# Optimization experiments

Hardware: AMD Instinct MI355X
Metric: run time of the kernel (lower is better)

The kernel has to match this reference:

```python
import jax, jax.numpy as jnp
import numpy as np

N_NODES = 20000  # number of batch nodes (static for segment ops)

def setup_inputs() -> dict:
    key = jax.random.key(0)
    N, E, V, D = N_NODES, 640000, 100000, 64
    ks = jax.random.split(key, 8)
    nodes = jax.random.randint(ks[0], (N,), 0, V)
    neigh_idx = jax.random.randint(ks[1], (E,), 0, V)
    seg_ids = jnp.sort(jax.random.randint(ks[2], (E,), 0, N))  # ragged degrees, sorted by node
    u2e = jax.random.normal(ks[3], (V, D), jnp.float32) * 0.02
    s1 = 1.0 / np.sqrt(2 * D)
    s2 = 1.0 / np.sqrt(D)
    att1_w = jax.random.uniform(ks[4], (2 * D, D), jnp.float32, -s1, s1)
    att1_b = jnp.zeros((D,), jnp.float32)
    att2_w = jax.random.uniform(ks[5], (D, D), jnp.float32, -s2, s2)
    att2_b = jnp.zeros((D,), jnp.float32)
    att3_w = jax.random.uniform(ks[6], (D, 1), jnp.float32, -s2, s2)
    att3_b = jnp.zeros((1,), jnp.float32)
    return dict(nodes=nodes, neigh_idx=neigh_idx, seg_ids=seg_ids, u2e=u2e,
                att1_w=att1_w, att1_b=att1_b, att2_w=att2_w, att2_b=att2_b,
                att3_w=att3_w, att3_b=att3_b)


def reference(nodes, neigh_idx, seg_ids, u2e, att1_w, att1_b, att2_w, att2_b, att3_w, att3_b):
    # Ragged per-node neighbor attention, flattened over all edges.
    e_u = u2e[neigh_idx]              # [E, D] neighbor embeddings
    u_rep = u2e[nodes][seg_ids]       # [E, D] center-node embedding broadcast per edge
    x = jnp.concatenate([e_u, u_rep], axis=1)            # [E, 2D]
    x = jax.nn.relu(x @ att1_w + att1_b)                  # [E, D]
    x = jax.nn.relu(x @ att2_w + att2_b)                  # [E, D]
    logits = (x @ att3_w + att3_b)[:, 0]                  # [E]
    # segment softmax over each node's neighbor set
    m = jax.ops.segment_max(logits, seg_ids, num_segments=N_NODES)
    m = jnp.where(jnp.isfinite(m), m, 0.0)                # guard empty segments
    ex = jnp.exp(logits - m[seg_ids])
    denom = jax.ops.segment_sum(ex, seg_ids, num_segments=N_NODES)
    att = ex / jnp.maximum(denom[seg_ids], 1e-9)          # [E]
    # attention-weighted sum of neighbor embeddings per node (e_u^T @ att_w per node)
    out = jax.ops.segment_sum(att[:, None] * e_u, seg_ids, num_segments=N_NODES)  # [N, D]
    return out
```

## Files before the change

### kernel.cpp

```cpp
#include <hip/hip_runtime.h>
#include <hip/hip_bf16.h>

typedef __attribute__((ext_vector_type(8))) short bf16x8;
typedef __attribute__((ext_vector_type(4))) float f32x4;

__device__ __forceinline__ unsigned short f2bf(float f) {
    unsigned x = __float_as_uint(f);
    unsigned r = (x + 0x7FFF + ((x >> 16) & 1)) >> 16;
    return (unsigned short)r;
}
__device__ __forceinline__ bf16x8 cvt8(const float* __restrict__ p) {
    bf16x8 r;
#pragma unroll
    for (int j = 0; j < 8; ++j) r[j] = (short)f2bf(p[j]);
    return r;
}
__device__ __forceinline__ unsigned pack_relu_bf16(unsigned yv, unsigned zv) {
    float lo = fmaxf(__uint_as_float(yv << 16) + __uint_as_float(zv << 16), 0.0f);
    float hi = fmaxf(__uint_as_float(yv & 0xFFFF0000u) + __uint_as_float(zv & 0xFFFF0000u), 0.0f);
    __hip_bfloat162 p = __float22bfloat162_rn(float2{lo, hi});
    return *(unsigned*)&p;
}

template <bool T1>
__launch_bounds__(256)
__global__ void conv_all_k(const float* __restrict__ u2e,
                           const int* __restrict__ nodes,
                           const int* __restrict__ segs,
                           const float* __restrict__ w1,
                           const float* __restrict__ w2,
                           const float* __restrict__ b1f,
                           unsigned short* __restrict__ yu,
                           unsigned short* __restrict__ z,
                           unsigned short* __restrict__ w2t,
                           int* __restrict__ seg_off,
                           float* __restrict__ zout,
                           float* __restrict__ den,
                           int V, int N, int E, int yblk, int zblk,
                           int ytiles, int ztiles) {
    __shared__ __align__(16) unsigned short w1l[64 * 72];
    const int bid = blockIdx.x;
    const int t = threadIdx.x;
    const int wid = t >> 6;
    const int lane = t & 63;
    const int q = lane >> 4;
    const int m15 = lane & 15;

    if (bid < yblk + zblk) {
        const bool isY = bid < yblk;
        const int kbase = isY ? 0 : 64;
        for (int u = t; u < 64 * 16; u += 256) {
            int k = u >> 4;
            int n4 = (u & 15) * 4;
            float4 v = *(const float4*)(w1 + (long)(kbase + k) * 64 + n4);
            w1l[(n4 + 0) * 72 + k] = f2bf(v.x);
            w1l[(n4 + 1) * 72 + k] = f2bf(v.y);
            w1l[(n4 + 2) * 72 + k] = f2bf(v.z);
            w1l[(n4 + 3) * 72 + k] = f2bf(v.w);
        }
        __syncthreads();

        bf16x8 wb0[4], wb1[4];
#pragma unroll
        for (int b = 0; b < 4; ++b) {
            const unsigned short* wr = w1l + (b * 16 + m15) * 72;
            wb0[b] = *(const bf16x8*)(wr + q * 8);
            wb1[b] = *(const bf16x8*)(wr + 32 + q * 8);
        }

        if (isY) {
            const int ystride = T1 ? 128 : 64;
            for (int tile = bid; tile < ytiles; tile += yblk) {
                const int wbase = tile * 64 + wid * 16;
                if (wbase >= V) continue;
                int row = min(wbase + m15, V - 1);
                const float* p = u2e + (long)row * 64;
                bf16x8 a0 = cvt8(p + q * 8);
                bf16x8 a1 = cvt8(p + 32 + q * 8);
                if (T1 && wbase + m15 < V) {
                    *(bf16x8*)(yu + (long)row * 128 + 64 + q * 8) = a0;
                    *(bf16x8*)(yu + (long)row * 128 + 96 + q * 8) = a1;
                }
                f32x4 acc[4];
#pragma unroll
                for (int b = 0; b < 4; ++b) {
                    acc[b] = (f32x4){0.f, 0.f, 0.f, 0.f};
                    acc[b] = __builtin_amdgcn_mfma_f32_16x16x32_bf16(a0, wb0[b], acc[b], 0, 0, 0);
                    acc[b] = __builtin_amdgcn_mfma_f32_16x16x32_bf16(a1, wb1[b], acc[b], 0, 0, 0);
                }
#pragma unroll
                for (int b = 0; b < 4; ++b)
#pragma unroll
                    for (int r = 0; r < 4; ++r) {
                        int rr = wbase + q * 4 + r;
                        if (rr < V) yu[(long)rr * ystride + b * 16 + m15] = f2bf(acc[b][r]);
                    }
            }
        } else {
            float b1v[4];
#pragma unroll
            for (int b = 0; b < 4; ++b) b1v[b] = b1f[b * 16 + m15];
            for (int tile = bid - yblk; tile < ztiles; tile += zblk) {
                const int wbase = tile * 64 + wid * 16;
                if (wbase >= N) continue;
                int nd = nodes[min(wbase + m15, N - 1)];
                const float* p = u2e + (long)nd * 64;
                bf16x8 a0 = cvt8(p + q * 8);
                bf16x8 a1 = cvt8(p + 32 + q * 8);
                f32x4 acc[4];
#pragma unroll
                for (int b = 0; b < 4; ++b) {
                    acc[b] = (f32x4){b1v[b], b1v[b], b1v[b], b1v[b]};
                    acc[b] = __builtin_amdgcn_mfma_f32_16x16x32_bf16(a0, wb0[b], acc[b], 0, 0, 0);
                    acc[b] = __builtin_amdgcn_mfma_f32_16x16x32_bf16(a1, wb1[b], acc[b], 0, 0, 0);
                }
#pragma unroll
                for (int b = 0; b < 4; ++b)
#pragma unroll
                    for (int r = 0; r < 4; ++r) {
                        int rr = wbase + q * 4 + r;
                        if (rr < N) z[(long)rr * 64 + b * 16 + m15] = f2bf(acc[b][r]);
                    }
            }
        }
    } else if (bid == yblk + zblk) {
        for (int i = t; i < 64 * 64; i += 256) {
            int k = i >> 6, n = i & 63;
            w2t[n * 64 + k] = f2bf(w2[i]);
        }
    } else {
        if (T1) {
            long zt = (long)(bid - yblk - zblk - 1) * 256 + t;
            long nth = (long)(gridDim.x - yblk - zblk - 1) * 256;
            f32x4 zz = (f32x4){0.f, 0.f, 0.f, 0.f};
            for (long i = zt; i < (long)N * 16; i += nth) ((f32x4*)zout)[i] = zz;
            for (long i = zt; i < (long)((N + 3) / 4); i += nth) ((f32x4*)den)[i] = zz;
        } else {
            int idx = (bid - yblk - zblk - 1) * 256 + t;
            if (idx > N) return;
            int l = 0, r = E;
            while (l < r) { int mid = (l + r) >> 1; if (segs[mid] < idx) l = mid + 1; else r = mid; }
            seg_off[idx] = l;
        }
    }
}

__launch_bounds__(256)
__global__ void fused_ea_k(const int* __restrict__ neigh,
                           const int* __restrict__ segs,
                           const unsigned short* __restrict__ yu,
                           const unsigned short* __restrict__ z,
                           const unsigned short* __restrict__ w2t,
                           const float* __restrict__ b2f,
                           const float* __restrict__ w3f,
                           const float* __restrict__ b3f,
                           float* __restrict__ outp,
                           float* __restrict__ den, int E) {
    const int wid = threadIdx.x >> 6;
    const int lane = threadIdx.x & 63;
    const int q = lane >> 4;
    const int m15 = lane & 15;
    const long base = ((long)blockIdx.x * 4 + wid) * 32;
    if (base >= E) return;

    int vi[2], sg[2];
    bool val[2];
#pragma unroll
    for (int g = 0; g < 2; ++g) {
        long e = base + g * 16 + m15;
        val[g] = e < E;
        int ec = (int)(val[g] ? e : (long)E - 1);
        vi[g] = neigh[ec];
        sg[g] = segs[ec];
    }
    bf16x8 y0[2], y1[2], u0[2], u1[2], zz0[2], zz1[2];
#pragma unroll
    for (int g = 0; g < 2; ++g) {
        const unsigned short* r = yu + (long)vi[g] * 128;
        y0[g] = *(const bf16x8*)(r + q * 8);
        y1[g] = *(const bf16x8*)(r + 32 + q * 8);
        u0[g] = *(const bf16x8*)(r + 64 + q * 16);
        u1[g] = *(const bf16x8*)(r + 64 + q * 16 + 8);
        const unsigned short* zr = z + (long)sg[g] * 64;
        zz0[g] = *(const bf16x8*)(zr + q * 8);
        zz1[g] = *(const bf16x8*)(zr + 32 + q * 8);
    }

    float b2v[4], w3v[4];
#pragma unroll
    for (int b = 0; b < 4; ++b) {
        b2v[b] = b2f[b * 16 + m15];
        w3v[b] = w3f[b * 16 + m15];
    }
    const float b3v = b3f[0];

    f32x4 acc[2][4];
#pragma unroll
    for (int g = 0; g < 2; ++g) {
        bf16x8 h0, h1;
#pragma unroll
        for (int j = 0; j < 4; ++j) {
            ((unsigned*)&h0)[j] = pack_relu_bf16(((unsigned*)&y0[g])[j], ((unsigned*)&zz0[g])[j]);
            ((unsigned*)&h1)[j] = pack_relu_bf16(((unsigned*)&y1[g])[j], ((unsigned*)&zz1[g])[j]);
        }
#pragma unroll
        for (int b = 0; b < 4; ++b) {
            acc[g][b] = (f32x4){b2v[b], b2v[b], b2v[b], b2v[b]};
            const bf16x8* wrow = (const bf16x8*)(w2t + (b * 16 + m15) * 64);
            acc[g][b] = __builtin_amdgcn_mfma_f32_16x16x32_bf16(h0, wrow[0 + q], acc[g][b], 0, 0, 0);
            acc[g][b] = __builtin_amdgcn_mfma_f32_16x16x32_bf16(h1, wrow[4 + q], acc[g][b], 0, 0, 0);
        }
    }

#pragma unroll
    for (int g = 0; g < 2; ++g) {
        float ev[4];
#pragma unroll
        for (int r = 0; r < 4; ++r) {
            float v = 0.0f;
#pragma unroll
            for (int b = 0; b < 4; ++b) v += fmaxf(acc[g][b][r], 0.0f) * w3v[b];
            v += __shfl_xor(v, 1);
            v += __shfl_xor(v, 2);
            v += __shfl_xor(v, 4);
            v += __shfl_xor(v, 8);
            ev[r] = __expf(v + b3v);
        }
        int rsel = m15 & 3;
        float exval = rsel == 0 ? ev[0] : (rsel == 1 ? ev[1] : (rsel == 2 ? ev[2] : ev[3]));
        float exm = __shfl(exval, ((m15 >> 2) << 4) | (m15 & 3));
        if (!val[g]) exm = 0.0f;

        float uc[16];
        const unsigned* du0 = (const unsigned*)&u0[g];
        const unsigned* du1 = (const unsigned*)&u1[g];
#pragma unroll
        for (int tt = 0; tt < 4; ++tt) {
            uc[2 * tt]         = __uint_as_float(du0[tt] << 16);
            uc[2 * tt + 1]     = __uint_as_float(du0[tt] & 0xFFFF0000u);
            uc[8 + 2 * tt]     = __uint_as_float(du1[tt] << 16);
            uc[8 + 2 * tt + 1] = __uint_as_float(du1[tt] & 0xFFFF0000u);
        }

        const int ndlo = __shfl(sg[g], 0);
        const int ndhi = __shfl(sg[g], 15);
        for (int nd = ndlo; nd <= ndhi; ++nd) {
            float sel = (sg[g] == nd) ? exm : 0.0f;
            float cs[16];
#pragma unroll
            for (int c = 0; c < 16; ++c) cs[c] = sel * uc[c];
            float c8[8];
            {
                const bool b = m15 & 1;
#pragma unroll
                for (int i = 0; i < 8; ++i) {
                    float keep = b ? cs[2 * i + 1] : cs[2 * i];
                    float send = b ? cs[2 * i] : cs[2 * i + 1];
                    c8[i] = keep + __shfl_xor(send, 1);
                }
            }
            float c4[4];
            {
                const bool b = m15 & 2;
#pragma unroll
                for (int i = 0; i < 4; ++i) {
                    float keep = b ? c8[2 * i + 1] : c8[2 * i];
                    float send = b ? c8[2 * i] : c8[2 * i + 1];
                    c4[i] = keep + __shfl_xor(send, 2);
                }
            }
            float c2[2];
            {
                const bool b = m15 & 4;
#pragma unroll
                for (int i = 0; i < 2; ++i) {
                    float keep = b ? c4[2 * i + 1] : c4[2 * i];
                    float send = b ? c4[2 * i] : c4[2 * i + 1];
                    c2[i] = keep + __shfl_xor(send, 4);
                }
            }
            float tot;
            {
                const bool b = m15 & 8;
                float keep = b ? c2[1] : c2[0];
                float send = b ? c2[0] : c2[1];
                tot = keep + __shfl_xor(send, 8);
            }
            atomicAdd(outp + (long)nd * 64 + lane, tot);
            float ds = sel;
            ds += __shfl_xor(ds, 1);
            ds += __shfl_xor(ds, 2);
            ds += __shfl_xor(ds, 4);
            ds += __shfl_xor(ds, 8);
            if (lane == 0) atomicAdd(den + nd, ds);
        }
    }
}

__launch_bounds__(256)
__global__ void div_k(float* __restrict__ out, const float* __restrict__ den, int N) {
    int i = blockIdx.x * 256 + threadIdx.x;
    if (i >= N * 16) return;
    float inv = 1.0f / fmaxf(den[i >> 4], 1e-9f);
    f32x4* p = (f32x4*)out + i;
    f32x4 v = *p;
    v[0] *= inv; v[1] *= inv; v[2] *= inv; v[3] *= inv;
    *p = v;
}

__launch_bounds__(256)
__global__ void logits2_k(const int* __restrict__ neigh,
                          const int* __restrict__ segs,
                          const unsigned short* __restrict__ Y,
                          const unsigned short* __restrict__ z,
                          const unsigned short* __restrict__ w2t,
                          const float* __restrict__ b2f,
                          const float* __restrict__ w3f, const float* __restrict__ b3f,
                          float* __restrict__ ex, int E) {
    const int wid = threadIdx.x >> 6;
    const int lane = threadIdx.x & 63;
    const int q = lane >> 4;
    const int m15 = lane & 15;
    const long base = ((long)blockIdx.x * 4 + wid) * 32;
    if (base >= E) return;

    int vi[2], sg[2];
#pragma unroll
    for (int g = 0; g < 2; ++g) {
        long e = base + g * 16 + m15;
        int ec = (int)(e < E ? e : (long)E - 1);
        vi[g] = neigh[ec];
        sg[g] = segs[ec];
    }
    bf16x8 y0[2], y1[2], zz0[2], zz1[2];
#pragma unroll
    for (int g = 0; g < 2; ++g) {
        const unsigned short* yr = Y + (long)vi[g] * 64;
        y0[g] = *(const bf16x8*)(yr + q * 8);
        y1[g] = *(const bf16x8*)(yr + 32 + q * 8);
        const unsigned short* zr = z + (long)sg[g] * 64;
        zz0[g] = *(const bf16x8*)(zr + q * 8);
        zz1[g] = *(const bf16x8*)(zr + 32 + q * 8);
    }

    float b2v[4], w3v[4];
#pragma unroll
    for (int b = 0; b < 4; ++b) {
        b2v[b] = b2f[b * 16 + m15];
        w3v[b] = w3f[b * 16 + m15];
    }

    f32x4 acc[2][4];
#pragma unroll
    for (int g = 0; g < 2; ++g) {
        bf16x8 h0, h1;
#pragma unroll
        for (int j = 0; j < 4; ++j) {
            ((unsigned*)&h0)[j] = pack_relu_bf16(((unsigned*)&y0[g])[j], ((unsigned*)&zz0[g])[j]);
            ((unsigned*)&h1)[j] = pack_relu_bf16(((unsigned*)&y1[g])[j], ((unsigned*)&zz1[g])[j]);
        }
#pragma unroll
        for (int b = 0; b < 4; ++b) {
            acc[g][b] = (f32x4){b2v[b], b2v[b], b2v[b], b2v[b]};
            const bf16x8* wrow = (const bf16x8*)(w2t + (b * 16 + m15) * 64);
            acc[g][b] = __builtin_amdgcn_mfma_f32_16x16x32_bf16(h0, wrow[0 + q], acc[g][b], 0, 0, 0);
            acc[g][b] = __builtin_amdgcn_mfma_f32_16x16x32_bf16(h1, wrow[4 + q], acc[g][b], 0, 0, 0);
        }
    }

    const float b3v = b3f[0];
#pragma unroll
    for (int g = 0; g < 2; ++g)
#pragma unroll
        for (int r = 0; r < 4; ++r) {
            float v = 0.0f;
#pragma unroll
            for (int b = 0; b < 4; ++b) v += fmaxf(acc[g][b][r], 0.0f) * w3v[b];
            v += __shfl_xor(v, 1);
            v += __shfl_xor(v, 2);
            v += __shfl_xor(v, 4);
            v += __shfl_xor(v, 8);
            long ee = base + g * 16 + q * 4 + r;
            if (m15 == r && ee < E) ex[ee] = __expf(v + b3v);
        }
}

__launch_bounds__(256)
__global__ void aggw_f32_k(const int* __restrict__ seg_off,
                           const int* __restrict__ neigh,
                           const float* __restrict__ u2e,
                           const float* __restrict__ ex,
                           float* __restrict__ out, int N) {
    const int wid = threadIdx.x >> 6;
    const int lane = threadIdx.x & 63;
    const int n = blockIdx.x * 4 + wid;
    if (n >= N) return;
    const int lo = seg_off[n];
    const int hi = seg_off[n + 1];
    const int slot = lane >> 3;
    const int cl = lane & 7;

    float a[8] = {0.f, 0.f, 0.f, 0.f, 0.f, 0.f, 0.f, 0.f};
    float s = 0.0f;

    for (int e = lo + slot; e < hi; e += 8) {
        float w = ex[e];
        int vi = neigh[e];
        s += w;
        const float* row = u2e + (long)vi * 64 + cl * 8;
        float4 v0 = *(const float4*)row;
        float4 v1 = *(const float4*)(row + 4);
        a[0] = fmaf(w, v0.x, a[0]); a[1] = fmaf(w, v0.y, a[1]);
        a[2] = fmaf(w, v0.z, a[2]); a[3] = fmaf(w, v0.w, a[3]);
        a[4] = fmaf(w, v1.x, a[4]); a[5] = fmaf(w, v1.y, a[5]);
        a[6] = fmaf(w, v1.z, a[6]); a[7] = fmaf(w, v1.w, a[7]);
    }
#pragma unroll
    for (int msk = 8; msk <= 32; msk <<= 1) {
        s += __shfl_xor(s, msk);
#pragma unroll
        for (int j = 0; j < 8; ++j) a[j] += __shfl_xor(a[j], msk);
    }
    if (slot == 0) {
        float inv = 1.0f / fmaxf(s, 1e-9f);
        float4 o0 = {a[0] * inv, a[1] * inv, a[2] * inv, a[3] * inv};
        float4 o1 = {a[4] * inv, a[5] * inv, a[6] * inv, a[7] * inv};
        float* op = out + (long)n * 64 + cl * 8;
        *(float4*)op = o0;
        *(float4*)(op + 4) = o1;
    }
}

__global__ void prep_bounds_k(const float* __restrict__ w1,
                              const float* __restrict__ w2,
                              const int* __restrict__ segs,
                              unsigned short* __restrict__ w1t,
                              unsigned short* __restrict__ w2t,
                              int* __restrict__ seg_off, int N, int E) {
    int t = threadIdx.x;
    if (blockIdx.x == 0) {
        for (int i = t; i < 128 * 64; i += 256) {
            int k = i >> 6, n = i & 63;
            w1t[n * 128 + k] = f2bf(w1[i]);
        }
        for (int i = t; i < 64 * 64; i += 256) {
            int k = i >> 6, n = i & 63;
            w2t[n * 64 + k] = f2bf(w2[i]);
        }
    } else {
        int idx = (blockIdx.x - 1) * 256 + t;
        if (idx > N) return;
        int l = 0, r = E;
        while (l < r) { int mid = (l + r) >> 1; if (segs[mid] < idx) l = mid + 1; else r = mid; }
        seg_off[idx] = l;
    }
}

__launch_bounds__(256)
__global__ void logits_fb_k(const int* __restrict__ nodes,
                            const int* __restrict__ neigh,
                            const int* __restrict__ segs,
                            const float* __restrict__ u2e,
                            const unsigned short* __restrict__ w1t,
                            const unsigned short* __restrict__ w2t,
                            const float* __restrict__ b1f, const float* __restrict__ b2f,
                            const float* __restrict__ w3f, const float* __restrict__ b3f,
                            float* __restrict__ ex, int E) {
    __shared__ __align__(16) unsigned short h1buf[4][16 * 72];
    const int wid = threadIdx.x >> 6;
    const int lane = threadIdx.x & 63;
    const int q = lane >> 4;
    const int m15 = lane & 15;
    const long base = ((long)blockIdx.x * 4 + wid) * 16;
    long ee0 = base + m15;
    int e = (int)(ee0 < E ? ee0 : (long)E - 1);
    int ni = neigh[e];
    int ctr = nodes[segs[e]];
    const float* eu = u2e + (long)ni * 64;
    const float* ur = u2e + (long)ctr * 64;
    bf16x8 a0 = cvt8(eu + q * 8), a1 = cvt8(eu + 32 + q * 8);
    bf16x8 a2 = cvt8(ur + q * 8), a3 = cvt8(ur + 32 + q * 8);
    f32x4 acc[4];
#pragma unroll
    for (int b = 0; b < 4; ++b) {
        float bvv = b1f[b * 16 + m15];
        acc[b] = (f32x4){bvv, bvv, bvv, bvv};
        const bf16x8* wrow = (const bf16x8*)(w1t + (b * 16 + m15) * 128);
        acc[b] = __builtin_amdgcn_mfma_f32_16x16x32_bf16(a0, wrow[0 + q], acc[b], 0, 0, 0);
        acc[b] = __builtin_amdgcn_mfma_f32_16x16x32_bf16(a1, wrow[4 + q], acc[b], 0, 0, 0);
        acc[b] = __builtin_amdgcn_mfma_f32_16x16x32_bf16(a2, wrow[8 + q], acc[b], 0, 0, 0);
        acc[b] = __builtin_amdgcn_mfma_f32_16x16x32_bf16(a3, wrow[12 + q], acc[b], 0, 0, 0);
    }
#pragma unroll
    for (int b = 0; b < 4; ++b)
#pragma unroll
        for (int r = 0; r < 4; ++r)
            h1buf[wid][(q * 4 + r) * 72 + b * 16 + m15] = f2bf(fmaxf(acc[b][r], 0.0f));
    const unsigned short* hrow = &h1buf[wid][m15 * 72];
    bf16x8 h0 = *(const bf16x8*)(hrow + q * 8);
    bf16x8 h1 = *(const bf16x8*)(hrow + 32 + q * 8);
    f32x4 acc2[4];
#pragma unroll
    for (int b = 0; b < 4; ++b) {
        float bvv = b2f[b * 16 + m15];
        acc2[b] = (f32x4){bvv, bvv, bvv, bvv};
        const bf16x8* wrow = (const bf16x8*)(w2t + (b * 16 + m15) * 64);
        acc2[b] = __builtin_amdgcn_mfma_f32_16x16x32_bf16(h0, wrow[0 + q], acc2[b], 0, 0, 0);
        acc2[b] = __builtin_amdgcn_mfma_f32_16x16x32_bf16(h1, wrow[4 + q], acc2[b], 0, 0, 0);
    }
    float b3v = b3f[0];
#pragma unroll
    for (int r = 0; r < 4; ++r) {
        float v = 0.0f;
#pragma unroll
        for (int b = 0; b < 4; ++b) v += fmaxf(acc2[b][r], 0.0f) * w3f[b * 16 + m15];
        v += __shfl_xor(v, 1);
        v += __shfl_xor(v, 2);
        v += __shfl_xor(v, 4);
        v += __shfl_xor(v, 8);
        long ee = base + q * 4 + r;
        if (m15 == r && ee < E) ex[ee] = __expf(v + b3v);
    }
}

extern "C" void kernel_launch(void* const* d_in, const int* in_sizes, int n_in,
                              void* d_out, int out_size, void* d_ws, size_t ws_size,
                              hipStream_t stream) {
    const int* nodes = (const int*)d_in[0];
    const int* neigh = (const int*)d_in[1];
    const int* segs  = (const int*)d_in[2];
    const float* u2e = (const float*)d_in[3];
    const float* w1  = (const float*)d_in[4];
    const float* b1  = (const float*)d_in[5];
    const float* w2  = (const float*)d_in[6];
    const float* b2  = (const float*)d_in[7];
    const float* w3  = (const float*)d_in[8];
    const float* b3  = (const float*)d_in[9];
    const int N = in_sizes[0];
    const int E = in_sizes[1];
    const long VD = in_sizes[3];
    const int V = (int)(VD / 64);

    char* ws = (char*)d_ws;
    size_t off = 0;
    auto alloc = [&](size_t bytes) { char* p = ws + off; off = (off + bytes + 255) & ~(size_t)255; return p; };
    float* ex = (float*)alloc((size_t)E * 4);
    int* seg_off = (int*)alloc((size_t)(N + 1) * 4);
    unsigned short* w1t = (unsigned short*)alloc(128 * 64 * 2);
    unsigned short* w2t = (unsigned short*)alloc(64 * 64 * 2);
    size_t need_min = off;
    unsigned short* Y = (unsigned short*)alloc((size_t)VD * 2);
    unsigned short* zb = (unsigned short*)alloc((size_t)N * 64 * 2);
    size_t need_t2 = off;
    unsigned short* yu = (unsigned short*)alloc((size_t)VD * 4);
    float* den = (float*)alloc((size_t)N * 4);
    size_t need_t1 = off;
    (void)need_min;

    float* out = (float*)d_out;

    const int ytiles = (V + 63) / 64;
    const int ztiles = (N + 63) / 64;
    const int yblk = ytiles < 640 ? ytiles : 640;
    const int zblk = ztiles < 160 ? ztiles : 160;
    const int bblocks = (N + 256) / 256;
    const int lblocks = ((E + 31) / 32 + 3) / 4;
    const int ablocks = (N + 3) / 4;
    const int ZBLK = 128;

    if (ws_size >= need_t1) {
        conv_all_k<true><<<yblk + zblk + 1 + ZBLK, 256, 0, stream>>>(
            u2e, nodes, segs, w1, w2, b1, yu, zb, w2t, nullptr, out, den,
            V, N, E, yblk, zblk, ytiles, ztiles);
        fused_ea_k<<<lblocks, 256, 0, stream>>>(
            neigh, segs, yu, zb, w2t, b2, w3, b3, out, den, E);
        div_k<<<(N * 16 + 255) / 256, 256, 0, stream>>>(out, den, N);
    } else if (ws_size >= need_t2) {
        conv_all_k<false><<<yblk + zblk + 1 + bblocks, 256, 0, stream>>>(
            u2e, nodes, segs, w1, w2, b1, Y, zb, w2t, seg_off, nullptr, nullptr,
            V, N, E, yblk, zblk, ytiles, ztiles);
        logits2_k<<<lblocks, 256, 0, stream>>>(neigh, segs, Y, zb, w2t, b2, w3, b3, ex, E);
        aggw_f32_k<<<ablocks, 256, 0, stream>>>(seg_off, neigh, u2e, ex, out, N);
    } else {
        const int pbblocks = 1 + (N + 256) / 256;
        prep_bounds_k<<<pbblocks, 256, 0, stream>>>(w1, w2, segs, w1t, w2t, seg_off, N, E);
        const int blocks1 = ((E + 15) / 16 + 3) / 4;
        logits_fb_k<<<blocks1, 256, 0, stream>>>(nodes, neigh, segs, u2e, w1t, w2t,
                                                 b1, b2, w3, b3, ex, E);
        aggw_f32_k<<<ablocks, 256, 0, stream>>>(seg_off, neigh, nullptr  == nullptr ? u2e : u2e, ex, out, N);
    }
}
```

Before: 149.2 us.

## Split interleaved Y/u buffer and aggregate with lane-per-feature sequential scan

```diff
diff --git a/kernel.cpp b/kernel.cpp
--- a/kernel.cpp
+++ b/kernel.cpp
@@ -30,7 +30,8 @@
                            const float* __restrict__ w1,
                            const float* __restrict__ w2,
                            const float* __restrict__ b1f,
-                           unsigned short* __restrict__ yu,
+                           unsigned short* __restrict__ Y,
+                           unsigned short* __restrict__ u2ebf,
                            unsigned short* __restrict__ z,
                            unsigned short* __restrict__ w2t,
                            int* __restrict__ seg_off,
@@ -69,7 +70,6 @@
         }
 
         if (isY) {
-            const int ystride = T1 ? 128 : 64;
             for (int tile = bid; tile < ytiles; tile += yblk) {
                 const int wbase = tile * 64 + wid * 16;
                 if (wbase >= V) continue;
@@ -78,8 +78,8 @@
                 bf16x8 a0 = cvt8(p + q * 8);
                 bf16x8 a1 = cvt8(p + 32 + q * 8);
                 if (T1 && wbase + m15 < V) {
-                    *(bf16x8*)(yu + (long)row * 128 + 64 + q * 8) = a0;
-                    *(bf16x8*)(yu + (long)row * 128 + 96 + q * 8) = a1;
+                    *(bf16x8*)(u2ebf + (long)row * 64 + q * 8) = a0;
+                    *(bf16x8*)(u2ebf + (long)row * 64 + 32 + q * 8) = a1;
                 }
                 f32x4 acc[4];
 #pragma unroll
@@ -93,7 +93,7 @@
 #pragma unroll
                     for (int r = 0; r < 4; ++r) {
                         int rr = wbase + q * 4 + r;
-                        if (rr < V) yu[(long)rr * ystride + b * 16 + m15] = f2bf(acc[b][r]);
+                        if (rr < V) Y[(long)rr * 64 + b * 16 + m15] = f2bf(acc[b][r]);
                     }
             }
         } else {
@@ -148,8 +148,9 @@
 __launch_bounds__(256)
 __global__ void fused_ea_k(const int* __restrict__ neigh,
                            const int* __restrict__ segs,
-                           const unsigned short* __restrict__ yu,
+                           const unsigned short* __restrict__ Y,
                            const unsigned short* __restrict__ z,
+                           const unsigned short* __restrict__ u2ebf,
                            const unsigned short* __restrict__ w2t,
                            const float* __restrict__ b2f,
                            const float* __restrict__ w3f,
@@ -173,14 +174,22 @@
         vi[g] = neigh[ec];
         sg[g] = segs[ec];
     }
-    bf16x8 y0[2], y1[2], u0[2], u1[2], zz0[2], zz1[2];
-#pragma unroll
-    for (int g = 0; g < 2; ++g) {
-        const unsigned short* r = yu + (long)vi[g] * 128;
-        y0[g] = *(const bf16x8*)(r + q * 8);
-        y1[g] = *(const bf16x8*)(r + 32 + q * 8);
-        u0[g] = *(const bf16x8*)(r + 64 + q * 16);
-        u1[g] = *(const bf16x8*)(r + 64 + q * 16 + 8);
+
+    unsigned short uv[2][16];
+#pragma unroll
+    for (int g = 0; g < 2; ++g)
+#pragma unroll
+        for (int j = 0; j < 16; ++j) {
+            int svi = __builtin_amdgcn_readlane(vi[g], j);
+            uv[g][j] = u2ebf[((long)svi << 6) + lane];
+        }
+
+    bf16x8 y0[2], y1[2], zz0[2], zz1[2];
+#pragma unroll
+    for (int g = 0; g < 2; ++g) {
+        const unsigned short* yr = Y + (long)vi[g] * 64;
+        y0[g] = *(const bf16x8*)(yr + q * 8);
+        y1[g] = *(const bf16x8*)(yr + 32 + q * 8);
         const unsigned short* zr = z + (long)sg[g] * 64;
         zz0[g] = *(const bf16x8*)(zr + q * 8);
         zz1[g] = *(const bf16x8*)(zr + 32 + q * 8);
@@ -212,6 +221,7 @@
         }
     }
 
+    float exm[2];
 #pragma unroll
     for (int g = 0; g < 2; ++g) {
         float ev[4];
@@ -228,73 +238,30 @@
         }
         int rsel = m15 & 3;
         float exval = rsel == 0 ? ev[0] : (rsel == 1 ? ev[1] : (rsel == 2 ? ev[2] : ev[3]));
-        float exm = __shfl(exval, ((m15 >> 2) << 4) | (m15 & 3));
-        if (!val[g]) exm = 0.0f;
-
-        float uc[16];
-        const unsigned* du0 = (const unsigned*)&u0[g];
-        const unsigned* du1 = (const unsigned*)&u1[g];
-#pragma unroll
-        for (int tt = 0; tt < 4; ++tt) {
-            uc[2 * tt]         = __uint_as_float(du0[tt] << 16);
-            uc[2 * tt + 1]     = __uint_as_float(du0[tt] & 0xFFFF0000u);
-            uc[8 + 2 * tt]     = __uint_as_float(du1[tt] << 16);
-            uc[8 + 2 * tt + 1] = __uint_as_float(du1[tt] & 0xFFFF0000u);
-        }
-
-        const int ndlo = __shfl(sg[g], 0);
-        const int ndhi = __shfl(sg[g], 15);
-        for (int nd = ndlo; nd <= ndhi; ++nd) {
-            float sel = (sg[g] == nd) ? exm : 0.0f;
-            float cs[16];
-#pragma unroll
-            for (int c = 0; c < 16; ++c) cs[c] = sel * uc[c];
-            float c8[8];
-            {
-                const bool b = m15 & 1;
-#pragma unroll
-                for (int i = 0; i < 8; ++i) {
-                    float keep = b ? cs[2 * i + 1] : cs[2 * i];
-                    float send = b ? cs[2 * i] : cs[2 * i + 1];
-                    c8[i] = keep + __shfl_xor(send, 1);
-                }
+        float em = __shfl(exval, ((m15 >> 2) << 4) | (m15 & 3));
+        exm[g] = val[g] ? em : 0.0f;
+    }
+
+    float a = 0.0f;
+    float ds = 0.0f;
+    int cur = __builtin_amdgcn_readlane(sg[0], 0);
+#pragma unroll
+    for (int g = 0; g < 2; ++g)
+#pragma unroll
+        for (int j = 0; j < 16; ++j) {
+            int ssg = __builtin_amdgcn_readlane(sg[g], j);
+            float sex = __uint_as_float(
+                (unsigned)__builtin_amdgcn_readlane(__float_as_uint(exm[g]), j));
+            if (ssg != cur) {
+                atomicAdd(outp + (long)cur * 64 + lane, a);
+                if (lane == 0) atomicAdd(den + cur, ds);
+                a = 0.0f; ds = 0.0f; cur = ssg;
             }
-            float c4[4];
-            {
-                const bool b = m15 & 2;
-#pragma unroll
-                for (int i = 0; i < 4; ++i) {
-                    float keep = b ? c8[2 * i + 1] : c8[2 * i];
-                    float send = b ? c8[2 * i] : c8[2 * i + 1];
-                    c4[i] = keep + __shfl_xor(send, 2);
-                }
-            }
-            float c2[2];
-            {
-                const bool b = m15 & 4;
-#pragma unroll
-                for (int i = 0; i < 2; ++i) {
-                    float keep = b ? c4[2 * i + 1] : c4[2 * i];
-                    float send = b ? c4[2 * i] : c4[2 * i + 1];
-                    c2[i] = keep + __shfl_xor(send, 4);
-                }
-            }
-            float tot;
-            {
-                const bool b = m15 & 8;
-                float keep = b ? c2[1] : c2[0];
-                float send = b ? c2[0] : c2[1];
-                tot = keep + __shfl_xor(send, 8);
-            }
-            atomicAdd(outp + (long)nd * 64 + lane, tot);
-            float ds = sel;
-            ds += __shfl_xor(ds, 1);
-            ds += __shfl_xor(ds, 2);
-            ds += __shfl_xor(ds, 4);
-            ds += __shfl_xor(ds, 8);
-            if (lane == 0) atomicAdd(den + nd, ds);
-        }
-    }
+            a = fmaf(sex, __uint_as_float((unsigned)uv[g][j] << 16), a);
+            ds += sex;
+        }
+    atomicAdd(outp + (long)cur * 64 + lane, a);
+    if (lane == 0) atomicAdd(den + cur, ds);
 }
 
 __launch_bounds__(256)
@@ -552,7 +519,7 @@
     unsigned short* Y = (unsigned short*)alloc((size_t)VD * 2);
     unsigned short* zb = (unsigned short*)alloc((size_t)N * 64 * 2);
     size_t need_t2 = off;
-    unsigned short* yu = (unsigned short*)alloc((size_t)VD * 4);
+    unsigned short* u2ebf = (unsigned short*)alloc((size_t)VD * 2);
     float* den = (float*)alloc((size_t)N * 4);
     size_t need_t1 = off;
     (void)need_min;
@@ -570,14 +537,14 @@
 
     if (ws_size >= need_t1) {
         conv_all_k<true><<<yblk + zblk + 1 + ZBLK, 256, 0, stream>>>(
-            u2e, nodes, segs, w1, w2, b1, yu, zb, w2t, nullptr, out, den,
+            u2e, nodes, segs, w1, w2, b1, Y, u2ebf, zb, w2t, nullptr, out, den,
             V, N, E, yblk, zblk, ytiles, ztiles);
         fused_ea_k<<<lblocks, 256, 0, stream>>>(
-            neigh, segs, yu, zb, w2t, b2, w3, b3, out, den, E);
+            neigh, segs, Y, zb, u2ebf, w2t, b2, w3, b3, out, den, E);
         div_k<<<(N * 16 + 255) / 256, 256, 0, stream>>>(out, den, N);
     } else if (ws_size >= need_t2) {
         conv_all_k<false><<<yblk + zblk + 1 + bblocks, 256, 0, stream>>>(
-            u2e, nodes, segs, w1, w2, b1, Y, zb, w2t, seg_off, nullptr, nullptr,
+            u2e, nodes, segs, w1, w2, b1, Y, nullptr, zb, w2t, seg_off, nullptr, nullptr,
             V, N, E, yblk, zblk, ytiles, ztiles);
         logits2_k<<<lblocks, 256, 0, stream>>>(neigh, segs, Y, zb, w2t, b2, w3, b3, ex, E);
         aggw_f32_k<<<ablocks, 256, 0, stream>>>(seg_off, neigh, u2e, ex, out, N);
@@ -587,6 +554,6 @@
         const int blocks1 = ((E + 15) / 16 + 3) / 4;
         logits_fb_k<<<blocks1, 256, 0, stream>>>(nodes, neigh, segs, u2e, w1t, w2t,
                                                  b1, b2, w3, b3, ex, E);
-        aggw_f32_k<<<ablocks, 256, 0, stream>>>(seg_off, neigh, nullptr  == nullptr ? u2e : u2e, ex, out, N);
-    }
-}
+        aggw_f32_k<<<ablocks, 256, 0, stream>>>(seg_off, neigh, u2e, ex, out, N);
+    }
+}
```

Result: no change. 147.4 us (-1.2%).
